# Optimization experiments

Measured on AMD Instinct MI355X. Metric: run time of the kernel, lower is better.

Reference implementation:

```python
import jax, jax.numpy as jnp
import numpy as np

N = 4096
D_IN = 512
D_H = 128
HEADS = 4
NEG_BIG = 1e10  # matches tf mask constant
LEAKY_ALPHA = 0.2  # tf.nn.leaky_relu default


def setup_inputs() -> dict:
    key = jax.random.key(0)
    ks = jax.random.split(key, 6)
    # 0/1 dense adjacency (faithful to tf.sparse.add producing dense 0/1 + mask)
    adjacency = jax.random.randint(ks[0], (N, N), 0, 2).astype(jnp.float32)
    # guarantee no empty rows (softmax over all -1e10 is degenerate)
    adjacency = adjacency.at[jnp.arange(N), jnp.arange(N)].set(1.0)
    input_feature = jax.random.normal(ks[1], (N, D_IN), dtype=jnp.float32)
    scale = 1.0 / np.sqrt(D_IN)
    kernels = jax.random.normal(ks[2], (HEADS, D_IN, D_H), dtype=jnp.float32) * scale
    biases = jnp.zeros((HEADS, D_H), dtype=jnp.float32)
    a_scale = 1.0 / np.sqrt(D_H)
    attn_self = jax.random.normal(ks[3], (HEADS, D_H), dtype=jnp.float32) * a_scale
    attn_neigh = jax.random.normal(ks[4], (HEADS, D_H), dtype=jnp.float32) * a_scale
    return {
        "adjacency": adjacency,
        "input_feature": input_feature,
        "kernels": kernels,
        "biases": biases,
        "attn_self": attn_self,
        "attn_neigh": attn_neigh,
    }


def reference(adjacency, input_feature, kernels, biases, attn_self, attn_neigh):
    # per-head feature projection: [H, N, D_h]
    feats = jnp.einsum("nd,hde->hne", input_feature, kernels)
    # additive attention logits
    a_s = jnp.einsum("hne,he->hn", feats, attn_self)   # [H, N]
    a_n = jnp.einsum("hne,he->hn", feats, attn_neigh)  # [H, N]
    dense = a_s[:, :, None] + a_n[:, None, :]          # [H, N, N]
    dense = jax.nn.leaky_relu(dense, negative_slope=LEAKY_ALPHA)
    mask = NEG_BIG * (adjacency - 1.0)                 # 0 where edge, -1e10 elsewhere
    dense = jax.nn.softmax(dense + mask[None, :, :], axis=-1)
    out = jnp.einsum("hnm,hme->hne", dense, feats) + biases[:, None, :]  # [H, N, D_h]
    # concat heads: [N, H*D_h]
    return jnp.transpose(out, (1, 0, 2)).reshape(out.shape[1], -1)
```

## Files before the change

kernel.cpp:

```cpp
#include <hip/hip_runtime.h>

#define NN 4096
#define DIN 512
#define DH 128
#define NH 4
#define JC 1024
#define NJC (NN/JC)
#define L2E 1.44269504f

typedef float f32x4 __attribute__((ext_vector_type(4)));
typedef _Float16 f16x8 __attribute__((ext_vector_type(8)));
typedef _Float16 f16x4 __attribute__((ext_vector_type(4)));
typedef _Float16 f16x2 __attribute__((ext_vector_type(2)));

__device__ __forceinline__ float leaky(float x){ return x > 0.f ? x : 0.2f*x; }

__global__ __launch_bounds__(256) void k_pack(
    const float* __restrict__ adj, unsigned int* __restrict__ bmg)
{
  __shared__ unsigned char nib[2][256];
  const int t = threadIdx.x;
  const size_t base = (size_t)blockIdx.x * 8192;
  #pragma unroll
  for (int it=0; it<8; ++it){
    const size_t fb = base + it*1024;
    f32x4 v = *(const f32x4*)&adj[fb + t*4];
    unsigned nb = (v[0]>0.5f?1u:0u)|(v[1]>0.5f?2u:0u)|(v[2]>0.5f?4u:0u)|(v[3]>0.5f?8u:0u);
    const int buf = it&1;
    nib[buf][t] = (unsigned char)nb;
    __syncthreads();
    if (t < 32){
      unsigned long long x = *(const unsigned long long*)&nib[buf][t*8];
      x &= 0x0F0F0F0F0F0F0F0FULL;
      x = (x | (x>>4))  & 0x00FF00FF00FF00FFULL;
      x = (x | (x>>8))  & 0x0000FFFF0000FFFFULL;
      x = (x | (x>>16));
      bmg[fb/32 + t] = (unsigned int)x;
    }
  }
}

__global__ __launch_bounds__(256) void k_gemm1(
    const float* __restrict__ X, const float* __restrict__ Kw,
    const float* __restrict__ attn_s, const float* __restrict__ attn_n,
    _Float16* __restrict__ featsT, float* __restrict__ a_s, float* __restrict__ a_n)
{
  const int it = blockIdx.x, h = blockIdx.y;
  const int i0 = it*64;
  const int t = threadIdx.x, w = t>>6, lane = t&63;
  const int eoff = (w>>1)*64, ioff = (w&1)*32;
  const int lg = lane>>4, li = lane&15;

  __shared__ _Float16 KT[128][40];
  __shared__ _Float16 XT[64][40];
  __shared__ float red_s[2][2][2][16];
  __shared__ float red_n[2][2][2][16];

  f32x4 acc[4][2] = {};

  for (int ks=0; ks<16; ++ks){
    const int d0 = ks*32;
    __syncthreads();
    #pragma unroll
    for (int q=0;q<4;q++){
      int f = t + 256*q;
      int e = f & 127, dg = (f>>7)*4;
      f16x4 hv;
      #pragma unroll
      for (int k=0;k<4;k++)
        hv[k] = (_Float16)Kw[(h*DIN + d0 + dg + k)*DH + e];
      *(f16x4*)&KT[e][dg] = hv;
    }
    #pragma unroll
    for (int q=0;q<2;q++){
      int f = t + 256*q;
      int i = f>>3, s = (f&7)*4;
      f32x4 v = *(const f32x4*)&X[(i0+i)*DIN + d0 + s];
      f16x4 hv; hv[0]=(_Float16)v[0]; hv[1]=(_Float16)v[1];
      hv[2]=(_Float16)v[2]; hv[3]=(_Float16)v[3];
      *(f16x4*)&XT[i][s] = hv;
    }
    __syncthreads();
    f16x8 af[4], bf[2];
    #pragma unroll
    for (int ef=0; ef<4; ++ef) af[ef] = *(const f16x8*)&KT[eoff + ef*16 + li][lg*8];
    #pragma unroll
    for (int f2=0; f2<2; ++f2) bf[f2] = *(const f16x8*)&XT[ioff + f2*16 + li][lg*8];
    #pragma unroll
    for (int ef=0; ef<4; ++ef)
      #pragma unroll
      for (int f2=0; f2<2; ++f2)
        acc[ef][f2] = __builtin_amdgcn_mfma_f32_16x16x32_f16(af[ef], bf[f2], acc[ef][f2], 0,0,0);
  }

  float ps[2] = {0,0}, pn[2] = {0,0};
  #pragma unroll
  for (int ef=0; ef<4; ++ef){
    #pragma unroll
    for (int r=0;r<4;r++){
      int e = eoff + ef*16 + lg*4 + r;
      float as_e = attn_s[h*DH + e];
      float an_e = attn_n[h*DH + e];
      #pragma unroll
      for (int f2=0; f2<2; ++f2){
        int irow = i0 + ioff + f2*16 + li;
        float v = acc[ef][f2][r];
        featsT[(h*DH + e)*NN + irow] = (_Float16)v;
        ps[f2] += v*as_e; pn[f2] += v*an_e;
      }
    }
  }
  #pragma unroll
  for (int f2=0; f2<2; ++f2){
    ps[f2] += __shfl_xor(ps[f2], 16); ps[f2] += __shfl_xor(ps[f2], 32);
    pn[f2] += __shfl_xor(pn[f2], 16); pn[f2] += __shfl_xor(pn[f2], 32);
  }
  if (lane < 16){
    red_s[w>>1][w&1][0][lane] = ps[0]; red_s[w>>1][w&1][1][lane] = ps[1];
    red_n[w>>1][w&1][0][lane] = pn[0]; red_n[w>>1][w&1][1][lane] = pn[1];
  }
  __syncthreads();
  if (t < 64){
    int ih = t>>5, fb = (t>>4)&1, l2 = t&15;
    a_s[h*NN + i0 + t] = red_s[0][ih][fb][l2] + red_s[1][ih][fb][l2];
    a_n[h*NN + i0 + t] = red_n[0][ih][fb][l2] + red_n[1][ih][fb][l2];
  }
}

__global__ void k_amax(const float* __restrict__ a_n, float* __restrict__ Amax,
                       _Float16* __restrict__ EA_g, _Float16* __restrict__ GA_g){
  int h = blockIdx.x, t = threadIdx.x;
  float m = -3.4e38f;
  for (int i=t; i<NN; i+=256){
    float v = a_n[h*NN+i];
    m = fmaxf(m, v);
    EA_g[h*NN+i] = (_Float16)__builtin_exp2f(v*L2E);
    GA_g[h*NN+i] = (_Float16)__builtin_exp2f(0.2f*v*L2E);
  }
  #pragma unroll
  for (int s=1; s<64; s<<=1) m = fmaxf(m, __shfl_xor(m, s));
  __shared__ float sm[4];
  if ((t&63)==0) sm[t>>6] = m;
  __syncthreads();
  if (t==0) Amax[h] = fmaxf(fmaxf(sm[0],sm[1]), fmaxf(sm[2],sm[3]));
}

__global__ __launch_bounds__(256, 2) void k_pv(
    const unsigned int* __restrict__ bmg, const _Float16* __restrict__ featsT,
    const float* __restrict__ a_s, const float* __restrict__ Amax,
    const _Float16* __restrict__ EA_g, const _Float16* __restrict__ GA_g,
    _Float16* __restrict__ Opart, float* __restrict__ Dpart)
{
  const int it = blockIdx.x, h = blockIdx.y, jcI = blockIdx.z;
  const int i0 = it*128, j0 = jcI*JC;
  const int t = threadIdx.x, w = t>>6, lane = t&63;
  const int lg = lane>>4, li = lane&15;
  const int rg = w&1, eh = w>>1;

  __shared__ _Float16 ft[3][128*32];
  __shared__ _Float16 ea_s[JC], ga_s[JC];
  __shared__ unsigned char bm_s[128][144];

  if (t < 128){
    __builtin_amdgcn_global_load_lds(
        (const __attribute__((address_space(1))) void*)(EA_g + h*NN + j0 + t*8),
        (__attribute__((address_space(3))) void*)(&ea_s[t*8]), 16, 0, 0);
  } else {
    __builtin_amdgcn_global_load_lds(
        (const __attribute__((address_space(1))) void*)(GA_g + h*NN + j0 + (t-128)*8),
        (__attribute__((address_space(3))) void*)(&ga_s[(t-128)*8]), 16, 0, 0);
  }
  #pragma unroll
  for (int p=0;p<4;p++){
    int idx = p*256 + t;
    int r = idx>>3, c = idx&7;
    uint4 v = *(const uint4*)((const char*)bmg + (size_t)(i0+r)*(NN/8) + jcI*(JC/8) + c*16);
    *(uint4*)&bm_s[r][c*16] = v;
  }

  const float am = Amax[h];
  f16x2 Epk[4], Gpk[4];
  #pragma unroll
  for (int f=0;f<4;f++){
    float asf = a_s[h*NN + i0 + rg*64 + f*16 + li];
    float mf = leaky(asf + am);
    Epk[f][0] = Epk[f][1] = (_Float16)__builtin_exp2f((asf - mf)*L2E);
    Gpk[f][0] = Gpk[f][1] = (_Float16)__builtin_exp2f((0.2f*asf - mf)*L2E);
  }

  auto STAGE = [&](int buf, int js){
    #pragma unroll
    for (int q=0;q<2;q++){
      int idx = q*256 + t;
      int e = idx>>2, p = idx&3;
      int l = p ^ ((e ^ (e>>2)) & 3);
      __builtin_amdgcn_global_load_lds(
          (const __attribute__((address_space(1))) void*)(featsT + (size_t)(h*DH + e)*NN + j0 + js*32 + l*8),
          (__attribute__((address_space(3))) void*)(&ft[buf][idx*8]), 16, 0, 0);
    }
  };

  STAGE(0, 0);
  STAGE(1, 1);
  __syncthreads();

  f32x4 acc[4][4] = {};
  f32x4 accd[4] = {};
  f16x8 ones;
  #pragma unroll
  for (int q=0;q<8;q++) ones[q] = (_Float16)1.0f;

  const int fsw = (li ^ (li>>2)) & 3;
  const int slot = lg ^ fsw;

  for (int js=0; js<32; ++js){
    asm volatile("s_waitcnt vmcnt(2)" ::: "memory");
    __builtin_amdgcn_s_barrier();
    { int nst = js+2 < 32 ? js+2 : 31; STAGE((js+2)%3, nst); }

    const int cur = js%3;
    union {f16x8 v; f16x2 p[4];} ea, ga;
    ea.v = *(const f16x8*)&ea_s[js*32 + lg*8];
    ga.v = *(const f16x8*)&ga_s[js*32 + lg*8];

    f16x8 bfr[4];
    #pragma unroll
    for (int ef=0; ef<4; ++ef){
      int row = eh*64 + ef*16 + li;
      bfr[ef] = *(const f16x8*)&ft[cur][row*32 + slot*8];
    }

    f16x8 af[4];
    #pragma unroll
    for (int f=0; f<4; ++f){
      unsigned b = (*(const unsigned*)&bm_s[rg*64 + f*16 + li][js*4]) >> (lg*8);
      union {f16x8 v; f16x2 p[4];} A;
      #pragma unroll
      for (int p2=0; p2<4; ++p2){
        f16x2 wv = __builtin_elementwise_max(Epk[f]*ea.p[p2], Gpk[f]*ga.p[p2]);
        int mlo = ((int)(b << (31-2*p2))) >> 31;
        int mhi = ((int)(b << (30-2*p2))) >> 31;
        unsigned m = ((unsigned)mlo & 0xFFFFu) | ((unsigned)mhi & 0xFFFF0000u);
        A.p[p2] = __builtin_bit_cast(f16x2,
                    (unsigned)(__builtin_bit_cast(unsigned, wv) & m));
      }
      af[f] = A.v;
    }

    __builtin_amdgcn_s_setprio(1);
    #pragma unroll
    for (int f=0; f<4; ++f){
      #pragma unroll
      for (int ef=0; ef<4; ++ef)
        acc[f][ef] = __builtin_amdgcn_mfma_f32_16x16x32_f16(af[f], bfr[ef], acc[f][ef], 0,0,0);
      accd[f] = __builtin_amdgcn_mfma_f32_16x16x32_f16(af[f], ones, accd[f], 0,0,0);
    }
    __builtin_amdgcn_s_setprio(0);
  }

  const size_t chb = (size_t)(jcI*4 + h)*NN;
  #pragma unroll
  for (int f=0; f<4; ++f){
    const int rbase = i0 + rg*64 + f*16;
    if (li == 0 && eh == 0)
      *(f32x4*)&Dpart[chb + rbase + lg*4] = accd[f];
    #pragma unroll
    for (int ef=0; ef<4; ++ef)
      #pragma unroll
      for (int r=0; r<4; ++r)
        Opart[(size_t)(chb + rbase + lg*4 + r)*DH + eh*64 + ef*16 + li]
            = (_Float16)acc[f][ef][r];
  }
}

__global__ __launch_bounds__(256) void k_out(
    const _Float16* __restrict__ Opart, const float* __restrict__ Dpart,
    const float* __restrict__ bias, float* __restrict__ out)
{
  int gid = blockIdx.x*256 + threadIdx.x;
  int base = gid*4;
  int i = base >> 9;
  int he = base & 511;
  int h = he >> 7;
  int e = he & 127;
  float n0=0,n1=0,n2=0,n3=0, den=0;
  #pragma unroll
  for (int jc=0; jc<NJC; ++jc){
    int ch = (jc*4+h)*NN + i;
    f16x4 v = *(const f16x4*)(Opart + (size_t)ch*DH + e);
    n0 += (float)v[0]; n1 += (float)v[1]; n2 += (float)v[2]; n3 += (float)v[3];
    den += Dpart[ch];
  }
  float inv = 1.f/den;
  f32x4 b4 = *(const f32x4*)&bias[he];
  f32x4 o; o[0]=n0*inv+b4[0]; o[1]=n1*inv+b4[1]; o[2]=n2*inv+b4[2]; o[3]=n3*inv+b4[3];
  *(f32x4*)&out[base] = o;
}

extern "C" void kernel_launch(void* const* d_in, const int* in_sizes, int n_in,
                              void* d_out, int out_size, void* d_ws, size_t ws_size,
                              hipStream_t stream)
{
  const float* adj   = (const float*)d_in[0];
  const float* X     = (const float*)d_in[1];
  const float* Kw    = (const float*)d_in[2];
  const float* bias  = (const float*)d_in[3];
  const float* atn_s = (const float*)d_in[4];
  const float* atn_n = (const float*)d_in[5];
  float* out = (float*)d_out;

  char* ws = (char*)d_ws;
  _Float16* featsT = (_Float16*)ws;
  unsigned int* bmg = (unsigned int*)(ws + ((size_t)4<<20));
  float* a_s  = (float*)(ws + (size_t)6*1024*1024);
  float* a_n  = a_s + NH*NN;
  float* Amax = a_n + NH*NN;
  _Float16* EA_g = (_Float16*)(Amax + 64);
  _Float16* GA_g = EA_g + NH*NN;
  float* Dpart = (float*)(GA_g + NH*NN);
  _Float16* Opart = (_Float16*)(Dpart + NJC*NH*NN);

  hipLaunchKernelGGL(k_pack, dim3(2048), dim3(256), 0, stream, adj, bmg);
  hipLaunchKernelGGL(k_gemm1, dim3(64,4), dim3(256), 0, stream,
                     X, Kw, atn_s, atn_n, featsT, a_s, a_n);
  hipLaunchKernelGGL(k_amax, dim3(4), dim3(256), 0, stream, a_n, Amax, EA_g, GA_g);
  hipLaunchKernelGGL(k_pv, dim3(32,4,NJC), dim3(256), 0, stream,
                     bmg, featsT, a_s, Amax, EA_g, GA_g, Opart, Dpart);
  hipLaunchKernelGGL(k_out, dim3(2048), dim3(256), 0, stream,
                     Opart, Dpart, bias, out);
}
```

Measured before the change: 78.75 us.

## Use per-wave double-buffered staging in k_pv, halve J-chunk, shuffle-based adjacency packing

In k_pv each wave now stages its own 64-row feature tile into a private double buffer, so the per-iteration block-wide barrier is no longer needed. The J chunk shrinks to 512, which doubles the grid and the number of partial outputs, and the launch-bounds occupancy hint rises to 3. k_pack now builds each bitmask word with cross-lane shuffles instead of LDS plus __syncthreads. The trade-offs are that the two waves sharing an eh half load the same feature rows, more partial-sum traffic goes to k_out, and the wave-private buffer reuse depends on wait-count ordering.

```diff
diff --git a/kernel.cpp b/kernel.cpp
--- a/kernel.cpp
+++ b/kernel.cpp
@@ -4,8 +4,9 @@
 #define DIN 512
 #define DH 128
 #define NH 4
-#define JC 1024
+#define JC 512
 #define NJC (NN/JC)
+#define JSTEPS (JC/32)
 #define L2E 1.44269504f
 
 typedef float f32x4 __attribute__((ext_vector_type(4)));
@@ -18,25 +19,17 @@
 __global__ __launch_bounds__(256) void k_pack(
     const float* __restrict__ adj, unsigned int* __restrict__ bmg)
 {
-  __shared__ unsigned char nib[2][256];
-  const int t = threadIdx.x;
-  const size_t base = (size_t)blockIdx.x * 8192;
-  #pragma unroll
-  for (int it=0; it<8; ++it){
-    const size_t fb = base + it*1024;
-    f32x4 v = *(const f32x4*)&adj[fb + t*4];
+  const int t = threadIdx.x, lane = t&63, w = t>>6;
+  const int wid = blockIdx.x*4 + w;
+  #pragma unroll
+  for (int it=0; it<16; ++it){
+    const size_t base = ((size_t)it*4096 + wid)*256;
+    f32x4 v = *(const f32x4*)&adj[base + lane*4];
     unsigned nb = (v[0]>0.5f?1u:0u)|(v[1]>0.5f?2u:0u)|(v[2]>0.5f?4u:0u)|(v[3]>0.5f?8u:0u);
-    const int buf = it&1;
-    nib[buf][t] = (unsigned char)nb;
-    __syncthreads();
-    if (t < 32){
-      unsigned long long x = *(const unsigned long long*)&nib[buf][t*8];
-      x &= 0x0F0F0F0F0F0F0F0FULL;
-      x = (x | (x>>4))  & 0x00FF00FF00FF00FFULL;
-      x = (x | (x>>8))  & 0x0000FFFF0000FFFFULL;
-      x = (x | (x>>16));
-      bmg[fb/32 + t] = (unsigned int)x;
-    }
+    unsigned x = nb | ((unsigned)__shfl_xor((int)nb, 1) << 4);
+    x = (x & 0xFFu)   | ((unsigned)__shfl_xor((int)x, 2) << 8);
+    x = (x & 0xFFFFu) | ((unsigned)__shfl_xor((int)x, 4) << 16);
+    if ((lane&7)==0) bmg[base/32 + (lane>>3)] = x;
   }
 }
 
@@ -145,7 +138,7 @@
   if (t==0) Amax[h] = fmaxf(fmaxf(sm[0],sm[1]), fmaxf(sm[2],sm[3]));
 }
 
-__global__ __launch_bounds__(256, 2) void k_pv(
+__global__ __launch_bounds__(256, 3) void k_pv(
     const unsigned int* __restrict__ bmg, const _Float16* __restrict__ featsT,
     const float* __restrict__ a_s, const float* __restrict__ Amax,
     const _Float16* __restrict__ EA_g, const _Float16* __restrict__ GA_g,
@@ -157,23 +150,23 @@
   const int lg = lane>>4, li = lane&15;
   const int rg = w&1, eh = w>>1;
 
-  __shared__ _Float16 ft[3][128*32];
+  __shared__ _Float16 ft[2][4][64*32];
   __shared__ _Float16 ea_s[JC], ga_s[JC];
-  __shared__ unsigned char bm_s[128][144];
-
-  if (t < 128){
+  __shared__ unsigned char bm_s[128][80];
+
+  if (t < 64){
     __builtin_amdgcn_global_load_lds(
         (const __attribute__((address_space(1))) void*)(EA_g + h*NN + j0 + t*8),
         (__attribute__((address_space(3))) void*)(&ea_s[t*8]), 16, 0, 0);
-  } else {
+  } else if (t < 128){
     __builtin_amdgcn_global_load_lds(
-        (const __attribute__((address_space(1))) void*)(GA_g + h*NN + j0 + (t-128)*8),
-        (__attribute__((address_space(3))) void*)(&ga_s[(t-128)*8]), 16, 0, 0);
-  }
-  #pragma unroll
-  for (int p=0;p<4;p++){
+        (const __attribute__((address_space(1))) void*)(GA_g + h*NN + j0 + (t-64)*8),
+        (__attribute__((address_space(3))) void*)(&ga_s[(t-64)*8]), 16, 0, 0);
+  }
+  #pragma unroll
+  for (int p=0;p<2;p++){
     int idx = p*256 + t;
-    int r = idx>>3, c = idx&7;
+    int r = idx>>2, c = idx&3;
     uint4 v = *(const uint4*)((const char*)bmg + (size_t)(i0+r)*(NN/8) + jcI*(JC/8) + c*16);
     *(uint4*)&bm_s[r][c*16] = v;
   }
@@ -189,19 +182,18 @@
   }
 
   auto STAGE = [&](int buf, int js){
-    #pragma unroll
-    for (int q=0;q<2;q++){
-      int idx = q*256 + t;
-      int e = idx>>2, p = idx&3;
-      int l = p ^ ((e ^ (e>>2)) & 3);
+    _Float16* dst = &ft[buf][w][0];
+    #pragma unroll
+    for (int q=0;q<4;q++){
+      int el = q*16 + (lane>>2);
+      int l = (lane&3) ^ (((lane>>2) ^ (lane>>4)) & 3);
       __builtin_amdgcn_global_load_lds(
-          (const __attribute__((address_space(1))) void*)(featsT + (size_t)(h*DH + e)*NN + j0 + js*32 + l*8),
-          (__attribute__((address_space(3))) void*)(&ft[buf][idx*8]), 16, 0, 0);
+          (const __attribute__((address_space(1))) void*)(featsT + (size_t)(h*DH + eh*64 + el)*NN + j0 + js*32 + l*8),
+          (__attribute__((address_space(3))) void*)(dst + q*512), 16, 0, 0);
     }
   };
 
   STAGE(0, 0);
-  STAGE(1, 1);
   __syncthreads();
 
   f32x4 acc[4][4] = {};
@@ -210,25 +202,23 @@
   #pragma unroll
   for (int q=0;q<8;q++) ones[q] = (_Float16)1.0f;
 
-  const int fsw = (li ^ (li>>2)) & 3;
-  const int slot = lg ^ fsw;
-
-  for (int js=0; js<32; ++js){
-    asm volatile("s_waitcnt vmcnt(2)" ::: "memory");
-    __builtin_amdgcn_s_barrier();
-    { int nst = js+2 < 32 ? js+2 : 31; STAGE((js+2)%3, nst); }
-
-    const int cur = js%3;
+  const int slot = lg ^ ((li ^ (li>>2)) & 3);
+
+  int buf = 0;
+  for (int js=0; js<JSTEPS; ++js){
+    { int nst = js+1 < JSTEPS ? js+1 : JSTEPS-1; STAGE(buf^1, nst); }
+    __builtin_amdgcn_sched_barrier(0);
+    asm volatile("s_waitcnt vmcnt(4)" ::: "memory");
+    __builtin_amdgcn_sched_barrier(0);
+
     union {f16x8 v; f16x2 p[4];} ea, ga;
     ea.v = *(const f16x8*)&ea_s[js*32 + lg*8];
     ga.v = *(const f16x8*)&ga_s[js*32 + lg*8];
 
     f16x8 bfr[4];
     #pragma unroll
-    for (int ef=0; ef<4; ++ef){
-      int row = eh*64 + ef*16 + li;
-      bfr[ef] = *(const f16x8*)&ft[cur][row*32 + slot*8];
-    }
+    for (int ef=0; ef<4; ++ef)
+      bfr[ef] = *(const f16x8*)&ft[buf][w][(ef*16+li)*32 + slot*8];
 
     f16x8 af[4];
     #pragma unroll
@@ -256,6 +246,7 @@
       accd[f] = __builtin_amdgcn_mfma_f32_16x16x32_f16(af[f], ones, accd[f], 0,0,0);
     }
     __builtin_amdgcn_s_setprio(0);
+    buf ^= 1;
   }
 
   const size_t chb = (size_t)(jcI*4 + h)*NN;
@@ -320,7 +311,7 @@
   float* Dpart = (float*)(GA_g + NH*NN);
   _Float16* Opart = (_Float16*)(Dpart + NJC*NH*NN);
 
-  hipLaunchKernelGGL(k_pack, dim3(2048), dim3(256), 0, stream, adj, bmg);
+  hipLaunchKernelGGL(k_pack, dim3(1024), dim3(256), 0, stream, adj, bmg);
   hipLaunchKernelGGL(k_gemm1, dim3(64,4), dim3(256), 0, stream,
                      X, Kw, atn_s, atn_n, featsT, a_s, a_n);
   hipLaunchKernelGGL(k_amax, dim3(4), dim3(256), 0, stream, a_n, Amax, EA_g, GA_g);
```

Measured after the change: 81.49 us. 1.03x slower.
